# Performance work log

Measured on AMD Instinct MI355X. Metric: run time of the kernel, lower is better.

## Reference

```python
import jax, jax.numpy as jnp
import numpy as np

D = 1024; H = 8; QLR = 384; KVLR = 256; NOPE = 128; ROPE = 64; VD = 128
E = 8; TOPK = 2; INTER = 512; NSH = 2; B = 2; T = 2048
QKD = NOPE + ROPE  # 192


def _rms(x, w, eps=1e-6):
    return x * jax.lax.rsqrt(jnp.mean(x * x, axis=-1, keepdims=True) + eps) * w


def _rope(x, cos, sin):
    # x: [B,T,h,ROPE]; pairs are consecutive elements (torch view(...,-1,2)).
    x0 = x[..., 0::2]
    x1 = x[..., 1::2]
    c = cos[None, :, None, :]
    s = sin[None, :, None, :]
    y0 = x0 * c - x1 * s
    y1 = x0 * s + x1 * c
    return jnp.stack([y0, y1], axis=-1).reshape(x.shape)


def setup_inputs() -> dict:
    key = jax.random.key(0)
    ks = jax.random.split(key, 12)
    def w(k, shape, scale=0.02):
        return jax.random.normal(k, shape, dtype=jnp.float32) * scale
    inv = 1.0 / (10000.0 ** (jnp.arange(0, ROPE, 2, dtype=jnp.float32) / ROPE))
    ang = jnp.arange(T, dtype=jnp.float32)[:, None] * inv[None, :]  # [T, ROPE//2]
    return {
        "x": jax.random.normal(ks[0], (B, T, D), dtype=jnp.float32),
        "freqs_cos": jnp.cos(ang),
        "freqs_sin": jnp.sin(ang),
        "rmsn1_w": jnp.ones((D,), jnp.float32),
        "rmsn2_w": jnp.ones((D,), jnp.float32),
        "latent_w": w(ks[1], (D, QLR + KVLR + ROPE)),
        "q_norm_w": jnp.ones((QLR,), jnp.float32),
        "q_up_w": w(ks[2], (QLR, H * QKD)),
        "kv_norm_w": jnp.ones((KVLR,), jnp.float32),
        "kv_up_w": w(ks[3], (KVLR, H * (NOPE + VD))),
        "c_proj_w": w(ks[4], (D, D)),
        "gate_w": w(ks[5], (D, E)),
        "sh_w1": w(ks[6], (D, INTER * NSH)),
        "sh_w2": w(ks[7], (INTER * NSH, D)),
        "sh_w3": w(ks[8], (D, INTER * NSH)),
        "e_w1": w(ks[9], (E, D, INTER)),
        "e_w2": w(ks[10], (E, INTER, D)),
        "e_w3": w(ks[11], (E, D, INTER)),
    }


def reference(x, freqs_cos, freqs_sin, rmsn1_w, rmsn2_w, latent_w, q_norm_w,
              q_up_w, kv_norm_w, kv_up_w, c_proj_w, gate_w, sh_w1, sh_w2,
              sh_w3, e_w1, e_w2, e_w3):
    Bx, Tx, _ = x.shape
    # ---- MLA attention ----
    h = _rms(x, rmsn1_w)
    lat = h @ latent_w
    q_l, kv_l, k_r = jnp.split(lat, [QLR, QLR + KVLR], axis=-1)
    q = (_rms(q_l, q_norm_w) @ q_up_w).reshape(Bx, Tx, H, QKD)
    q_n, q_r = q[..., :NOPE], q[..., NOPE:]
    q_r = _rope(q_r, freqs_cos, freqs_sin)
    q = jnp.concatenate([q_n, q_r], axis=-1)  # [B,T,H,QKD]
    kv = (_rms(kv_l, kv_norm_w) @ kv_up_w).reshape(Bx, Tx, H, NOPE + VD)
    k_n, v = kv[..., :NOPE], kv[..., NOPE:]
    k_r = _rope(k_r[:, :, None, :], freqs_cos, freqs_sin)
    k_r = jnp.broadcast_to(k_r, (Bx, Tx, H, ROPE))
    k = jnp.concatenate([k_n, k_r], axis=-1)
    scale = 1.0 / jnp.sqrt(jnp.float32(QKD))
    scores = jnp.einsum('bqhd,bkhd->bhqk', q, k) * scale
    causal = jnp.tril(jnp.ones((Tx, Tx), dtype=bool))
    scores = jnp.where(causal, scores, jnp.finfo(scores.dtype).min)
    attn = jax.nn.softmax(scores, axis=-1)
    y = jnp.einsum('bhqk,bkhd->bqhd', attn, v).reshape(Bx, Tx, D)
    x = x + y @ c_proj_w
    # ---- DeepSeekMoE ----
    h2 = _rms(x, rmsn2_w).reshape(-1, D)  # [N, D]
    y_sh = (jax.nn.silu(h2 @ sh_w1) * (h2 @ sh_w3)) @ sh_w2
    scores_g = jax.nn.softmax(h2 @ gate_w, axis=-1)  # [N, E]
    w_top, idx = jax.lax.top_k(scores_g, TOPK)  # weights == gathered original scores
    # combine weights per expert (route_scale = 1.0)
    cw = jnp.sum(jax.nn.one_hot(idx, E, dtype=h2.dtype) * w_top[..., None], axis=1)  # [N, E]
    h1 = jnp.einsum('nd,edi->eni', h2, e_w1)
    h3 = jnp.einsum('nd,edi->eni', h2, e_w3)
    out_e = jnp.einsum('eni,eid->end', jax.nn.silu(h1) * h3, e_w2)  # [E, N, D]
    y_moe = y_sh + jnp.einsum('end,ne->nd', out_e, cw)
    return x + y_moe.reshape(Bx, Tx, D)
```

## Files before the change

### kernel.cpp

```cpp
#include <hip/hip_runtime.h>
#include <hip/hip_bf16.h>
#include <math.h>

#define D_ 1024
#define H_ 8
#define QLR_ 384
#define KVLR_ 256
#define NOPE_ 128
#define ROPE_ 64
#define VD_ 128
#define E_ 8
#define INTER_ 512
#define B_ 2
#define T_ 2048
#define QKD_ 192
#define NTOK (B_*T_)
#define LSTR 4608
#define MAXMB 72

typedef __attribute__((ext_vector_type(8))) short short8;
typedef __attribute__((ext_vector_type(4))) float f32x4;

__device__ __forceinline__ unsigned short f2bf(float f) {
  union { float f; unsigned u; } v; v.f = f;
  return (unsigned short)((v.u + 0x7FFFu + ((v.u >> 16) & 1u)) >> 16);
}
__device__ __forceinline__ float bf2f(unsigned short h) {
  union { unsigned u; float f; } v; v.u = ((unsigned)h) << 16;
  return v.f;
}

#define GLD16(SRC, DST) __builtin_amdgcn_global_load_lds( \
    (__attribute__((address_space(1))) void*)(SRC), \
    (__attribute__((address_space(3))) void*)(DST), 16, 0, 0)

#define DPPF(v, ctrl) __int_as_float(__builtin_amdgcn_update_dpp(0, __float_as_int(v), ctrl, 0xF, 0xF, true))
__device__ __forceinline__ float dppmax16(float v) {
  v = fmaxf(v, DPPF(v, 0xB1));
  v = fmaxf(v, DPPF(v, 0x4E));
  v = fmaxf(v, DPPF(v, 0x124));
  v = fmaxf(v, DPPF(v, 0x128));
  return v;
}
__device__ __forceinline__ float dppsum16(float v) {
  v += DPPF(v, 0xB1);
  v += DPPF(v, 0x4E);
  v += DPPF(v, 0x124);
  v += DPPF(v, 0x128);
  return v;
}

__global__ __launch_bounds__(256) void transpose_f32_bf16(
    const float* __restrict__ in, unsigned short* __restrict__ out,
    int R, int C, size_t inBS, size_t outBS) {
  __shared__ float tile[32][33];
  const float* inp = in + (size_t)blockIdx.z * inBS;
  unsigned short* outp = out + (size_t)blockIdx.z * outBS;
  int c0 = blockIdx.x * 32, r0 = blockIdx.y * 32;
  int tx = threadIdx.x & 31, ty = threadIdx.x >> 5;
  #pragma unroll
  for (int i = 0; i < 4; ++i) {
    int rr = ty + i * 8;
    tile[rr][tx] = inp[(size_t)(r0 + rr) * C + c0 + tx];
  }
  __syncthreads();
  #pragma unroll
  for (int i = 0; i < 4; ++i) {
    int rr = ty + i * 8;
    outp[(size_t)(c0 + rr) * R + r0 + tx] = f2bf(tile[tx][rr]);
  }
}

__global__ __launch_bounds__(256) void transpose_pair(
    const float* __restrict__ in1, const float* __restrict__ in3,
    unsigned short* __restrict__ out, int K, int C1, size_t inBS, size_t outBS) {
  __shared__ float tile[32][33];
  int z = blockIdx.z; int bat = z >> 1; int f = (z & 1) * 16;
  const float* src = ((z & 1) ? in3 : in1) + (size_t)bat * inBS;
  unsigned short* o = out + (size_t)bat * outBS;
  int c0 = blockIdx.x * 32, r0 = blockIdx.y * 32;
  int tx = threadIdx.x & 31, ty = threadIdx.x >> 5;
  #pragma unroll
  for (int i = 0; i < 4; ++i) {
    int rr = ty + i * 8;
    tile[rr][tx] = src[(size_t)(r0 + rr) * C1 + c0 + tx];
  }
  __syncthreads();
  #pragma unroll
  for (int i = 0; i < 4; ++i) {
    int cc = ty + i * 8;
    int c = c0 + cc;
    int n = ((c >> 4) << 5) + (c & 15) + f;
    o[(size_t)n * K + r0 + tx] = f2bf(tile[tx][cc]);
  }
}

template<typename TI>
__global__ __launch_bounds__(256) void rms_to_bf16(
    const TI* __restrict__ src, int stride, int off, const float* __restrict__ w,
    unsigned short* __restrict__ out, int Dd, int outStride) {
  int row = blockIdx.x;
  const TI* xr = src + (size_t)row * stride + off;
  float ss = 0.f;
  for (int i = threadIdx.x; i < Dd; i += 256) {
    float v;
    if constexpr (sizeof(TI) == 2) v = bf2f((unsigned short)xr[i]); else v = (float)xr[i];
    ss += v * v;
  }
  for (int o = 1; o < 64; o <<= 1) ss += __shfl_xor(ss, o);
  __shared__ float red[4];
  if ((threadIdx.x & 63) == 0) red[threadIdx.x >> 6] = ss;
  __syncthreads();
  float tot = red[0] + red[1] + red[2] + red[3];
  float inv = 1.f / sqrtf(tot / Dd + 1e-6f);
  for (int i = threadIdx.x; i < Dd; i += 256) {
    float v;
    if constexpr (sizeof(TI) == 2) v = bf2f((unsigned short)xr[i]); else v = (float)xr[i];
    out[(size_t)row * outStride + i] = f2bf(v * inv * w[i]);
  }
}

__global__ __launch_bounds__(256) void lat_post(
    const unsigned short* __restrict__ lat, const float* __restrict__ qw,
    const float* __restrict__ kw, const float* __restrict__ fc, const float* __restrict__ fs,
    unsigned short* __restrict__ qn, unsigned short* __restrict__ kvn,
    unsigned short* __restrict__ kr) {
  int row = blockIdx.x, tid = threadIdx.x;
  int lane = tid & 63, wv = tid >> 6;
  const unsigned short* lr = lat + (size_t)row * 768;
  float s1 = 0.f, s2 = 0.f;
  for (int i = tid; i < QLR_; i += 256) { float v = bf2f(lr[i]); s1 += v * v; }
  { float v = bf2f(lr[QLR_ + tid]); s2 = v * v; }
  for (int o = 1; o < 64; o <<= 1) { s1 += __shfl_xor(s1, o); s2 += __shfl_xor(s2, o); }
  __shared__ float red[8];
  if (lane == 0) { red[wv] = s1; red[4 + wv] = s2; }
  __syncthreads();
  float inv1 = 1.f / sqrtf((red[0] + red[1] + red[2] + red[3]) / QLR_ + 1e-6f);
  float inv2 = 1.f / sqrtf((red[4] + red[5] + red[6] + red[7]) / KVLR_ + 1e-6f);
  for (int i = tid; i < QLR_; i += 256)
    qn[(size_t)row * QLR_ + i] = f2bf(bf2f(lr[i]) * inv1 * qw[i]);
  kvn[(size_t)row * KVLR_ + tid] = f2bf(bf2f(lr[QLR_ + tid]) * inv2 * kw[tid]);
  if (tid < 32) {
    int t = row & (T_ - 1);
    float c = fc[t * 32 + tid], s = fs[t * 32 + tid];
    float x0 = bf2f(lr[640 + 2 * tid]), x1 = bf2f(lr[640 + 2 * tid + 1]);
    kr[(size_t)row * ROPE_ + 2 * tid]     = f2bf(x0 * c - x1 * s);
    kr[(size_t)row * ROPE_ + 2 * tid + 1] = f2bf(x0 * s + x1 * c);
  }
}

template<int MODE>
__global__ __launch_bounds__(256) void gemm_bf16(
    const unsigned short* __restrict__ A, const unsigned short* __restrict__ Bt,
    void* __restrict__ Cv, int M, int N, int K,
    const float* __restrict__ addv) {
  __shared__ __align__(16) unsigned short As[128 * 32];
  __shared__ __align__(16) unsigned short Bs[128 * 32];
  const int tid = threadIdx.x;
  const int lane = tid & 63, wave = tid >> 6;
  const int wm = wave >> 1, wn = wave & 1;
  const int bm = blockIdx.y * 128, bn = blockIdx.x * 128;
  const int r = lane & 15, g = lane >> 4;

  f32x4 acc[4][4];
  #pragma unroll
  for (int i = 0; i < 4; ++i)
    #pragma unroll
    for (int j = 0; j < 4; ++j) acc[i][j] = (f32x4)0.f;

  const int rl0 = wave * 16 + (lane >> 2);
  const int rl1 = rl0 + 64;
  const int kc = (lane & 3) * 8;
  char* AsB = (char*)As; char* BsB = (char*)Bs;

  for (int k0 = 0; k0 < K; k0 += 32) {
    GLD16(A + (size_t)(bm + rl0) * K + k0 + kc, AsB + wave * 1024);
    GLD16(A + (size_t)(bm + rl1) * K + k0 + kc, AsB + (wave + 4) * 1024);
    GLD16(Bt + (size_t)(bn + rl0) * K + k0 + kc, BsB + wave * 1024);
    GLD16(Bt + (size_t)(bn + rl1) * K + k0 + kc, BsB + (wave + 4) * 1024);
    __syncthreads();
    short8 af[4], bfr[4];
    #pragma unroll
    for (int mi = 0; mi < 4; ++mi)
      af[mi] = *(const short8*)(As + (wm * 64 + mi * 16 + r) * 32 + g * 8);
    #pragma unroll
    for (int nj = 0; nj < 4; ++nj)
      bfr[nj] = *(const short8*)(Bs + (wn * 64 + nj * 16 + r) * 32 + g * 8);
    #pragma unroll
    for (int mi = 0; mi < 4; ++mi)
      #pragma unroll
      for (int nj = 0; nj < 4; ++nj)
        acc[mi][nj] = __builtin_amdgcn_mfma_f32_16x16x32_bf16(af[mi], bfr[nj], acc[mi][nj], 0, 0, 0);
    __syncthreads();
  }

  const int orow0 = wm * 64 + g * 4;
  const int ocol0 = bn + wn * 64 + r;
  #pragma unroll
  for (int mi = 0; mi < 4; ++mi) {
    #pragma unroll
    for (int reg = 0; reg < 4; ++reg) {
      int mrow = bm + orow0 + mi * 16 + reg;
      if (MODE == 4) {
        unsigned short* C = (unsigned short*)Cv;
        size_t bas2 = (size_t)mrow * (N >> 1) + ((bn + wn * 64) >> 1) + r;
        #pragma unroll
        for (int p = 0; p < 2; ++p) {
          float a = acc[mi][2 * p][reg], b3 = acc[mi][2 * p + 1][reg];
          C[bas2 + p * 16] = f2bf((a / (1.f + __expf(-a))) * b3);
        }
      } else {
        size_t bas = (size_t)mrow * N + ocol0;
        if (MODE == 0) {
          unsigned short* C = (unsigned short*)Cv;
          #pragma unroll
          for (int nj = 0; nj < 4; ++nj) C[bas + nj * 16] = f2bf(acc[mi][nj][reg]);
        } else if (MODE == 1) {
          float* C = (float*)Cv;
          #pragma unroll
          for (int nj = 0; nj < 4; ++nj) C[bas + nj * 16] = acc[mi][nj][reg] + addv[bas + nj * 16];
        } else {
          float* C = (float*)Cv;
          #pragma unroll
          for (int nj = 0; nj < 4; ++nj) C[bas + nj * 16] += acc[mi][nj][reg];
        }
      }
    }
  }
}

__global__ __launch_bounds__(256) void gemm_moe13(
    const unsigned short* __restrict__ A, const unsigned short* __restrict__ W,
    unsigned short* __restrict__ Cb,
    const int* __restrict__ lists, const int* __restrict__ map, const int* __restrict__ sbase) {
  int mb = map[blockIdx.y];
  if (mb < 0) return;
  const int e = mb >> 16, ib = mb & 0xFFFF;
  __shared__ __align__(16) unsigned short As[128 * 32];
  __shared__ __align__(16) unsigned short Bs[128 * 32];
  const int tid = threadIdx.x, lane = tid & 63, wave = tid >> 6;
  const int wm = wave >> 1, wn = wave & 1;
  const int bn = blockIdx.x * 128;
  const int r = lane & 15, g = lane >> 4;

  f32x4 acc[4][4];
  #pragma unroll
  for (int i = 0; i < 4; ++i)
    #pragma unroll
    for (int j = 0; j < 4; ++j) acc[i][j] = (f32x4)0.f;

  const int rl0 = wave * 16 + (lane >> 2), rl1 = rl0 + 64;
  const int kc = (lane & 3) * 8;
  int t0 = lists[e * LSTR + ib * 128 + rl0]; if (t0 < 0) t0 = 0;
  int t1 = lists[e * LSTR + ib * 128 + rl1]; if (t1 < 0) t1 = 0;
  const unsigned short* Wb = W + (size_t)e * 1024 * 1024;
  char* AsB = (char*)As; char* BsB = (char*)Bs;

  for (int k0 = 0; k0 < 1024; k0 += 32) {
    GLD16(A + (size_t)t0 * 1024 + k0 + kc, AsB + wave * 1024);
    GLD16(A + (size_t)t1 * 1024 + k0 + kc, AsB + (wave + 4) * 1024);
    GLD16(Wb + (size_t)(bn + rl0) * 1024 + k0 + kc, BsB + wave * 1024);
    GLD16(Wb + (size_t)(bn + rl1) * 1024 + k0 + kc, BsB + (wave + 4) * 1024);
    __syncthreads();
    short8 af[4], bfr[4];
    #pragma unroll
    for (int mi = 0; mi < 4; ++mi)
      af[mi] = *(const short8*)(As + (wm * 64 + mi * 16 + r) * 32 + g * 8);
    #pragma unroll
    for (int nj = 0; nj < 4; ++nj)
      bfr[nj] = *(const short8*)(Bs + (wn * 64 + nj * 16 + r) * 32 + g * 8);
    #pragma unroll
    for (int mi = 0; mi < 4; ++mi)
      #pragma unroll
      for (int nj = 0; nj < 4; ++nj)
        acc[mi][nj] = __builtin_amdgcn_mfma_f32_16x16x32_bf16(af[mi], bfr[nj], acc[mi][nj], 0, 0, 0);
    __syncthreads();
  }
  const int sb = sbase[e] + ib * 128;
  const int hc = ((bn + wn * 64) >> 1) + r;
  #pragma unroll
  for (int mi = 0; mi < 4; ++mi)
    #pragma unroll
    for (int reg = 0; reg < 4; ++reg) {
      int srow = sb + wm * 64 + mi * 16 + g * 4 + reg;
      #pragma unroll
      for (int p = 0; p < 2; ++p) {
        float a = acc[mi][2 * p][reg], b3 = acc[mi][2 * p + 1][reg];
        Cb[(size_t)srow * 512 + hc + p * 16] = f2bf((a / (1.f + __expf(-a))) * b3);
      }
    }
}

__global__ __launch_bounds__(256) void gemm_moe2(
    const unsigned short* __restrict__ Am, const unsigned short* __restrict__ W,
    float* __restrict__ out,
    const int* __restrict__ lists, const int* __restrict__ map, const int* __restrict__ sbase,
    const float* __restrict__ cw) {
  int mb = map[blockIdx.y];
  if (mb < 0) return;
  const int e = mb >> 16, ib = mb & 0xFFFF;
  __shared__ __align__(16) unsigned short As[128 * 32];
  __shared__ __align__(16) unsigned short Bs[128 * 32];
  const int tid = threadIdx.x, lane = tid & 63, wave = tid >> 6;
  const int wm = wave >> 1, wn = wave & 1;
  const int bn = blockIdx.x * 128;
  const int r = lane & 15, g = lane >> 4;

  f32x4 acc[4][4];
  #pragma unroll
  for (int i = 0; i < 4; ++i)
    #pragma unroll
    for (int j = 0; j < 4; ++j) acc[i][j] = (f32x4)0.f;

  const int rl0 = wave * 16 + (lane >> 2), rl1 = rl0 + 64;
  const int kc = (lane & 3) * 8;
  const int sb = sbase[e] + ib * 128;
  const unsigned short* Wb = W + (size_t)e * 512 * 1024;
  char* AsB = (char*)As; char* BsB = (char*)Bs;

  for (int k0 = 0; k0 < 512; k0 += 32) {
    GLD16(Am + (size_t)(sb + rl0) * 512 + k0 + kc, AsB + wave * 1024);
    GLD16(Am + (size_t)(sb + rl1) * 512 + k0 + kc, AsB + (wave + 4) * 1024);
    GLD16(Wb + (size_t)(bn + rl0) * 512 + k0 + kc, BsB + wave * 1024);
    GLD16(Wb + (size_t)(bn + rl1) * 512 + k0 + kc, BsB + (wave + 4) * 1024);
    __syncthreads();
    short8 af[4], bfr[4];
    #pragma unroll
    for (int mi = 0; mi < 4; ++mi)
      af[mi] = *(const short8*)(As + (wm * 64 + mi * 16 + r) * 32 + g * 8);
    #pragma unroll
    for (int nj = 0; nj < 4; ++nj)
      bfr[nj] = *(const short8*)(Bs + (wn * 64 + nj * 16 + r) * 32 + g * 8);
    #pragma unroll
    for (int mi = 0; mi < 4; ++mi)
      #pragma unroll
      for (int nj = 0; nj < 4; ++nj)
        acc[mi][nj] = __builtin_amdgcn_mfma_f32_16x16x32_bf16(af[mi], bfr[nj], acc[mi][nj], 0, 0, 0);
    __syncthreads();
  }
  const int ocol0 = bn + wn * 64 + r;
  #pragma unroll
  for (int mi = 0; mi < 4; ++mi)
    #pragma unroll
    for (int reg = 0; reg < 4; ++reg) {
      int orow = wm * 64 + mi * 16 + g * 4 + reg;
      int tok = lists[e * LSTR + ib * 128 + orow];
      if (tok >= 0) {
        float wt = cw[(size_t)tok * E_ + e];
        #pragma unroll
        for (int nj = 0; nj < 4; ++nj)
          atomicAdd(out + (size_t)tok * 1024 + ocol0 + nj * 16, acc[mi][nj][reg] * wt);
      }
    }
}

__global__ void rope_q_bf16(unsigned short* __restrict__ q, const float* __restrict__ c_,
                            const float* __restrict__ s_) {
  int idx = blockIdx.x * blockDim.x + threadIdx.x;
  if (idx >= NTOK * H_ * 32) return;
  int i = idx & 31, h = (idx >> 5) & 7, n = idx >> 8;
  int t = n & (T_ - 1);
  float c = c_[t * 32 + i], s = s_[t * 32 + i];
  unsigned short* base = q + (size_t)n * (H_ * QKD_) + h * QKD_ + NOPE_;
  float x0 = bf2f(base[2 * i]), x1 = bf2f(base[2 * i + 1]);
  base[2 * i]     = f2bf(x0 * c - x1 * s);
  base[2 * i + 1] = f2bf(x0 * s + x1 * c);
}

__global__ __launch_bounds__(256) void vtrans(const unsigned short* __restrict__ kvb,
                                              unsigned short* __restrict__ vt) {
  __shared__ unsigned short tile[32][33];
  int bh = blockIdx.z; int b = bh >> 3, h = bh & 7;
  int t0 = blockIdx.x * 32, d0 = blockIdx.y * 32;
  int tx = threadIdx.x & 31, ty = threadIdx.x >> 5;
  #pragma unroll
  for (int i = 0; i < 4; ++i) {
    int row = ty + i * 8;
    tile[row][tx] = kvb[((size_t)(b * T_ + t0 + row) * H_ + h) * 256 + 128 + d0 + tx];
  }
  __syncthreads();
  #pragma unroll
  for (int i = 0; i < 4; ++i) {
    int row = ty + i * 8;
    vt[((size_t)bh * 128 + d0 + row) * T_ + t0 + tx] = tile[tx][row];
  }
}

#define AQ 64
#define AK 32
#define VP 40
__global__ __launch_bounds__(256) void attn_mfma(
    const unsigned short* __restrict__ q,
    const unsigned short* __restrict__ kv,
    const unsigned short* __restrict__ kr,
    const unsigned short* __restrict__ vt,
    unsigned short* __restrict__ y) {
  __shared__ __align__(16) unsigned short Qs[AQ * 192];
  __shared__ __align__(16) unsigned short Ks[AK * 192];
  __shared__ __align__(16) unsigned short Vl[128 * VP];
  __shared__ __align__(16) unsigned short Ps[4 * 16 * VP];
  const int tid = threadIdx.x, lane = tid & 63, wave = tid >> 6;
  const int r = lane & 15, g = lane >> 4;
  const int bh = blockIdx.y, b = bh >> 3, h = bh & 7;
  const int qt = gridDim.x - 1 - blockIdx.x;
  const int q0 = qt * AQ;
  const size_t bT = (size_t)b * T_;
  const unsigned short* vbase = vt + (size_t)bh * 128 * T_;
  char* QsB = (char*)Qs; char* KsB = (char*)Ks;

  #pragma unroll
  for (int it = 0; it < 6; ++it) {
    int c = tid + it * 256;
    int row = c / 24, c8 = c % 24;
    short8 v = *(const short8*)(q + ((bT + q0 + row) * H_ + h) * 192 + c8 * 8);
    *(short8*)(QsB + ((row * 384 + c8 * 16) ^ ((row & 7) << 4))) = v;
  }

  float m_i[4], l_i[4];
  f32x4 o[8];
  #pragma unroll
  for (int i = 0; i < 4; ++i) { m_i[i] = -1e30f; l_i[i] = 0.f; }
  #pragma unroll
  for (int cb = 0; cb < 8; ++cb) o[cb] = (f32x4)0.f;

  const float scale = 0.07216878364870322f;
  const int ntiles = q0 / AK + 2;

  short8 kreg[3], vreg[2];
  int krow[3], kcol[3];
  #pragma unroll
  for (int it = 0; it < 3; ++it) {
    int c = tid + it * 256;
    krow[it] = c / 24; kcol[it] = c % 24;
    kreg[it] = (kcol[it] < 16)
      ? *(const short8*)(kv + ((bT + krow[it]) * H_ + h) * 256 + kcol[it] * 8)
      : *(const short8*)(kr + (bT + krow[it]) * 64 + (kcol[it] - 16) * 8);
  }
  #pragma unroll
  for (int it = 0; it < 2; ++it) {
    int x = tid + it * 256;
    vreg[it] = *(const short8*)(vbase + (size_t)(x >> 2) * T_ + (x & 3) * 8);
  }

  for (int kt = 0; kt < ntiles; ++kt) {
    __syncthreads();
    #pragma unroll
    for (int it = 0; it < 3; ++it)
      *(short8*)(KsB + ((krow[it] * 384 + kcol[it] * 16) ^ ((krow[it] & 7) << 4))) = kreg[it];
    #pragma unroll
    for (int it = 0; it < 2; ++it) {
      int x = tid + it * 256;
      *(short8*)(Vl + (x >> 2) * VP + (x & 3) * 8) = vreg[it];
    }
    __syncthreads();

    if (kt + 1 < ntiles) {
      int k1 = (kt + 1) * AK;
      #pragma unroll
      for (int it = 0; it < 3; ++it)
        kreg[it] = (kcol[it] < 16)
          ? *(const short8*)(kv + ((bT + k1 + krow[it]) * H_ + h) * 256 + kcol[it] * 8)
          : *(const short8*)(kr + (bT + k1 + krow[it]) * 64 + (kcol[it] - 16) * 8);
      #pragma unroll
      for (int it = 0; it < 2; ++it) {
        int x = tid + it * 256;
        vreg[it] = *(const short8*)(vbase + (size_t)(x >> 2) * T_ + k1 + (x & 3) * 8);
      }
    }

    const int k0 = kt * AK;
    f32x4 sf0 = (f32x4)0.f, sf1 = (f32x4)0.f;
    {
      int qrow = wave * 16 + r;
      int qsw = (qrow & 7) << 4, ksw = (r & 7) << 4;
      #pragma unroll
      for (int kk = 0; kk < 6; ++kk) {
        short8 aq = *(const short8*)(QsB + ((qrow * 384 + kk * 64 + g * 16) ^ qsw));
        short8 b0 = *(const short8*)(KsB + ((r * 384 + kk * 64 + g * 16) ^ ksw));
        short8 b1 = *(const short8*)(KsB + (((16 + r) * 384 + kk * 64 + g * 16) ^ ksw));
        sf0 = __builtin_amdgcn_mfma_f32_16x16x32_bf16(aq, b0, sf0, 0, 0, 0);
        sf1 = __builtin_amdgcn_mfma_f32_16x16x32_bf16(aq, b1, sf1, 0, 0, 0);
      }
    }
    float fac[4];
    bool needs = false;
    #pragma unroll
    for (int reg = 0; reg < 4; ++reg) {
      float s0 = sf0[reg] * scale;
      float s1 = sf1[reg] * scale;
      int qp = q0 + wave * 16 + g * 4 + reg;
      if (k0 + r > qp) s0 = -1e30f;
      if (k0 + 16 + r > qp) s1 = -1e30f;
      float mt = dppmax16(fmaxf(s0, s1));
      float fc, mn;
      if (mt > m_i[reg] + 5.f) {
        mn = mt; fc = __expf(m_i[reg] - mn); m_i[reg] = mn; needs = true;
      } else { mn = m_i[reg]; fc = 1.f; }
      float e0 = __expf(s0 - mn), e1 = __expf(s1 - mn);
      float rs = dppsum16(e0 + e1);
      l_i[reg] = l_i[reg] * fc + rs;
      fac[reg] = fc;
      int prow = g * 4 + reg;
      Ps[wave * 16 * VP + prow * VP + r] = f2bf(e0);
      Ps[wave * 16 * VP + prow * VP + 16 + r] = f2bf(e1);
    }
    if (__any(needs)) {
      #pragma unroll
      for (int cb = 0; cb < 8; ++cb)
        #pragma unroll
        for (int reg = 0; reg < 4; ++reg) o[cb][reg] *= fac[reg];
    }
    short8 pa = *(const short8*)(Ps + wave * 16 * VP + r * VP + g * 8);
    #pragma unroll
    for (int cb = 0; cb < 8; ++cb) {
      short8 vb = *(const short8*)(Vl + (cb * 16 + r) * VP + g * 8);
      o[cb] = __builtin_amdgcn_mfma_f32_16x16x32_bf16(pa, vb, o[cb], 0, 0, 0);
    }
  }

  #pragma unroll
  for (int reg = 0; reg < 4; ++reg) {
    float inv = 1.f / l_i[reg];
    int nrow = q0 + wave * 16 + g * 4 + reg;
    size_t bas = (bT + nrow) * (size_t)D_ + h * VD_;
    #pragma unroll
    for (int cb = 0; cb < 8; ++cb)
      y[bas + cb * 16 + r] = f2bf(o[cb][reg] * inv);
  }
}

__global__ __launch_bounds__(256) void rms2_gate(
    const float* __restrict__ xo, const float* __restrict__ rw, const float* __restrict__ gw,
    unsigned short* __restrict__ h2b, float* __restrict__ cw) {
  int row = blockIdx.x, tid = threadIdx.x;
  int lane = tid & 63, wv = tid >> 6;
  const float* xr = xo + (size_t)row * D_;
  float v[4]; float ss = 0.f;
  #pragma unroll
  for (int j = 0; j < 4; ++j) { v[j] = xr[tid + j * 256]; ss += v[j] * v[j]; }
  for (int o = 1; o < 64; o <<= 1) ss += __shfl_xor(ss, o);
  __shared__ float red[4];
  if (lane == 0) red[wv] = ss;
  __syncthreads();
  float inv = 1.f / sqrtf((red[0] + red[1] + red[2] + red[3]) / D_ + 1e-6f);
  float a[E_] = {0, 0, 0, 0, 0, 0, 0, 0};
  #pragma unroll
  for (int j = 0; j < 4; ++j) {
    int i = tid + j * 256;
    float hv = v[j] * inv * rw[i];
    h2b[(size_t)row * D_ + i] = f2bf(hv);
    const float* wr = gw + (size_t)i * E_;
    #pragma unroll
    for (int e = 0; e < E_; ++e) a[e] += hv * wr[e];
  }
  #pragma unroll
  for (int e = 0; e < E_; ++e) {
    float t = a[e];
    for (int o = 1; o < 64; o <<= 1) t += __shfl_xor(t, o);
    a[e] = t;
  }
  __shared__ float ga[4][E_];
  if (lane == 0)
    #pragma unroll
    for (int e = 0; e < E_; ++e) ga[wv][e] = a[e];
  __syncthreads();
  if (tid == 0) {
    float lg[E_];
    #pragma unroll
    for (int e = 0; e < E_; ++e) lg[e] = ga[0][e] + ga[1][e] + ga[2][e] + ga[3][e];
    float mx = lg[0];
    #pragma unroll
    for (int e = 1; e < E_; ++e) mx = fmaxf(mx, lg[e]);
    float sum = 0.f; float p[E_];
    #pragma unroll
    for (int e = 0; e < E_; ++e) { p[e] = __expf(lg[e] - mx); sum += p[e]; }
    float is = 1.f / sum;
    int i1 = 0; float b1 = p[0];
    #pragma unroll
    for (int e = 1; e < E_; ++e) if (p[e] > b1) { b1 = p[e]; i1 = e; }
    int i2 = -1; float b2 = -1.f;
    #pragma unroll
    for (int e = 0; e < E_; ++e) if (e != i1 && p[e] > b2) { b2 = p[e]; i2 = e; }
    #pragma unroll
    for (int e = 0; e < E_; ++e)
      cw[(size_t)row * E_ + e] = (e == i1) ? b1 * is : (e == i2 ? b2 * is : 0.f);
  }
}

__global__ __launch_bounds__(256) void moe_build(const float* __restrict__ cw,
                                                 int* __restrict__ lists, int* __restrict__ counts) {
  int e = blockIdx.x, tid = threadIdx.x;
  int lane = tid & 63, wv = tid >> 6;
  __shared__ int wsum[4];
  __shared__ int base;
  if (tid == 0) base = 0;
  __syncthreads();
  for (int c0 = 0; c0 < NTOK; c0 += 256) {
    int tok = c0 + tid;
    bool f = cw[(size_t)tok * E_ + e] > 0.f;
    unsigned long long m = __ballot(f);
    int pos = __popcll(m & ((1ull << lane) - 1ull));
    if (lane == 0) wsum[wv] = __popcll(m);
    __syncthreads();
    int woff = base;
    #pragma unroll
    for (int w = 0; w < 4; ++w) if (w < wv) woff += wsum[w];
    if (f) lists[e * LSTR + woff + pos] = tok;
    __syncthreads();
    if (tid == 0) base += wsum[0] + wsum[1] + wsum[2] + wsum[3];
    __syncthreads();
  }
  int cnt = base;
  int padded = (cnt + 127) & ~127;
  for (int i2 = cnt + tid; i2 < padded; i2 += 256) lists[e * LSTR + i2] = -1;
  if (tid == 0) { counts[e] = cnt; counts[8 + e] = padded >> 7; }
}

__global__ void moe_finalize(const int* __restrict__ counts, int* __restrict__ map,
                             int* __restrict__ sbase) {
  if (threadIdx.x == 0 && blockIdx.x == 0) {
    int cum = 0;
    for (int e = 0; e < E_; ++e) {
      sbase[e] = cum * 128;
      int nb = counts[8 + e];
      for (int i = 0; i < nb; ++i) map[cum + i] = (e << 16) | i;
      cum += nb;
    }
    for (; cum < MAXMB; ++cum) map[cum] = -1;
  }
}

extern "C" void kernel_launch(void* const* d_in, const int* in_sizes, int n_in,
                              void* d_out, int out_size, void* d_ws, size_t ws_size,
                              hipStream_t stream) {
  const float* x        = (const float*)d_in[0];
  const float* fcos     = (const float*)d_in[1];
  const float* fsin     = (const float*)d_in[2];
  const float* rmsn1_w  = (const float*)d_in[3];
  const float* rmsn2_w  = (const float*)d_in[4];
  const float* latent_w = (const float*)d_in[5];
  const float* q_norm_w = (const float*)d_in[6];
  const float* q_up_w   = (const float*)d_in[7];
  const float* kv_norm_w= (const float*)d_in[8];
  const float* kv_up_w  = (const float*)d_in[9];
  const float* c_proj_w = (const float*)d_in[10];
  const float* gate_w   = (const float*)d_in[11];
  const float* sh_w1    = (const float*)d_in[12];
  const float* sh_w2    = (const float*)d_in[13];
  const float* sh_w3    = (const float*)d_in[14];
  const float* e_w1     = (const float*)d_in[15];
  const float* e_w2     = (const float*)d_in[16];
  const float* e_w3     = (const float*)d_in[17];
  float* out = (float*)d_out;

  char* base = (char*)d_ws;
  size_t off = 0;
  auto take = [&](size_t bytes) { char* p = base + off; off += (bytes + 255) & ~(size_t)255; return p; };
  unsigned short* Wlat  = (unsigned short*)take((size_t)768 * 1024 * 2);
  unsigned short* Wqup  = (unsigned short*)take((size_t)1536 * 384 * 2);
  unsigned short* Wkv   = (unsigned short*)take((size_t)2048 * 256 * 2);
  unsigned short* Wcp   = (unsigned short*)take((size_t)1024 * 1024 * 2);
  unsigned short* Wsh13 = (unsigned short*)take((size_t)2048 * 1024 * 2);
  unsigned short* Wsh2  = (unsigned short*)take((size_t)1024 * 1024 * 2);
  unsigned short* Wew13 = (unsigned short*)take((size_t)8 * 1024 * 1024 * 2);
  unsigned short* Wew2  = (unsigned short*)take((size_t)8 * 1024 * 512 * 2);
  float* cw             = (float*)take((size_t)NTOK * E_ * 4);
  int* lists            = (int*)take((size_t)E_ * LSTR * 4);
  int* counts           = (int*)take(64 * 4);
  int* map              = (int*)take(MAXMB * 4);
  int* sbase            = (int*)take(E_ * 4);
  unsigned short* Vtg   = (unsigned short*)take((size_t)16 * 128 * T_ * 2);
  unsigned short* kr    = (unsigned short*)take((size_t)NTOK * 64 * 2);

  size_t actStart = off;
  size_t aoff = actStart;
  auto takeA = [&](size_t bytes) { char* p = base + aoff; aoff += (bytes + 255) & ~(size_t)255; return p; };
  unsigned short* h_bf = (unsigned short*)takeA((size_t)NTOK * 1024 * 2);
  unsigned short* lat  = (unsigned short*)takeA((size_t)NTOK * 768 * 2);
  unsigned short* qn   = (unsigned short*)takeA((size_t)NTOK * 384 * 2);
  unsigned short* kvn  = (unsigned short*)takeA((size_t)NTOK * 256 * 2);
  unsigned short* qq   = (unsigned short*)takeA((size_t)NTOK * 1536 * 2);
  unsigned short* kvb  = (unsigned short*)takeA((size_t)NTOK * 2048 * 2);
  unsigned short* y    = (unsigned short*)takeA((size_t)NTOK * 1024 * 2);

  size_t coff = actStart;
  auto takeC = [&](size_t bytes) { char* p = base + coff; coff += (bytes + 255) & ~(size_t)255; return p; };
  unsigned short* h2b  = (unsigned short*)takeC((size_t)NTOK * 1024 * 2);
  unsigned short* t1m  = (unsigned short*)takeC((size_t)NTOK * 1024 * 2);
  unsigned short* ehm  = (unsigned short*)takeC((size_t)9216 * 512 * 2);

  dim3 blk(256);

  transpose_f32_bf16<<<dim3(22, 32, 1), blk, 0, stream>>>(latent_w, Wlat, 1024, 704, 0, 0);
  transpose_f32_bf16<<<dim3(48, 12, 1), blk, 0, stream>>>(q_up_w, Wqup, 384, 1536, 0, 0);
  transpose_f32_bf16<<<dim3(64, 8, 1), blk, 0, stream>>>(kv_up_w, Wkv, 256, 2048, 0, 0);
  transpose_f32_bf16<<<dim3(32, 32, 1), blk, 0, stream>>>(c_proj_w, Wcp, 1024, 1024, 0, 0);
  transpose_f32_bf16<<<dim3(32, 32, 1), blk, 0, stream>>>(sh_w2, Wsh2, 1024, 1024, 0, 0);
  transpose_pair<<<dim3(32, 32, 2), blk, 0, stream>>>(sh_w1, sh_w3, Wsh13, 1024, 1024, 0, 0);
  transpose_pair<<<dim3(16, 32, 16), blk, 0, stream>>>(e_w1, e_w3, Wew13, 1024, 512,
      (size_t)1024 * 512, (size_t)1024 * 1024);
  transpose_f32_bf16<<<dim3(32, 16, 8), blk, 0, stream>>>(e_w2, Wew2, 512, 1024,
      (size_t)512 * 1024, (size_t)1024 * 512);

  rms_to_bf16<float><<<NTOK, blk, 0, stream>>>(x, D_, 0, rmsn1_w, h_bf, D_, D_);
  gemm_bf16<0><<<dim3(6, 32), blk, 0, stream>>>(h_bf, Wlat, lat, NTOK, 768, 1024, nullptr);
  lat_post<<<NTOK, blk, 0, stream>>>(lat, q_norm_w, kv_norm_w, fcos, fsin, qn, kvn, kr);
  gemm_bf16<0><<<dim3(12, 32), blk, 0, stream>>>(qn, Wqup, qq, NTOK, 1536, 384, nullptr);
  rope_q_bf16<<<(NTOK * H_ * 32 + 255) / 256, blk, 0, stream>>>(qq, fcos, fsin);
  gemm_bf16<0><<<dim3(16, 32), blk, 0, stream>>>(kvn, Wkv, kvb, NTOK, 2048, 256, nullptr);
  vtrans<<<dim3(T_/32, 4, 16), blk, 0, stream>>>(kvb, Vtg);
  attn_mfma<<<dim3(T_ / AQ, B_ * H_), blk, 0, stream>>>(qq, kvb, kr, Vtg, y);
  gemm_bf16<1><<<dim3(8, 32), blk, 0, stream>>>(y, Wcp, out, NTOK, 1024, 1024, x);
  rms2_gate<<<NTOK, blk, 0, stream>>>(out, rmsn2_w, gate_w, h2b, cw);
  moe_build<<<E_, blk, 0, stream>>>(cw, lists, counts);
  moe_finalize<<<1, 64, 0, stream>>>(counts, map, sbase);
  gemm_bf16<4><<<dim3(16, 32), blk, 0, stream>>>(h2b, Wsh13, t1m, NTOK, 2048, 1024, nullptr);
  gemm_bf16<2><<<dim3(8, 32), blk, 0, stream>>>(t1m, Wsh2, out, NTOK, 1024, 1024, nullptr);
  gemm_moe13<<<dim3(8, MAXMB), blk, 0, stream>>>(h2b, Wew13, ehm, lists, map, sbase);
  gemm_moe2<<<dim3(8, MAXMB), blk, 0, stream>>>(ehm, Wew2, out, lists, map, sbase, cw);
}
```

Before: 411.0 us.

## Fuse V transpose into kv GEMM, fuse q RoPE into attention, tune softmax

```diff
diff --git a/kernel.cpp b/kernel.cpp
--- a/kernel.cpp
+++ b/kernel.cpp
@@ -20,6 +20,7 @@
 
 typedef __attribute__((ext_vector_type(8))) short short8;
 typedef __attribute__((ext_vector_type(4))) float f32x4;
+typedef __attribute__((ext_vector_type(4))) unsigned short us4;
 
 __device__ __forceinline__ unsigned short f2bf(float f) {
   union { float f; unsigned u; } v; v.f = f;
@@ -153,7 +154,7 @@
 __global__ __launch_bounds__(256) void gemm_bf16(
     const unsigned short* __restrict__ A, const unsigned short* __restrict__ Bt,
     void* __restrict__ Cv, int M, int N, int K,
-    const float* __restrict__ addv) {
+    const float* __restrict__ addv, unsigned short* __restrict__ vtg) {
   __shared__ __align__(16) unsigned short As[128 * 32];
   __shared__ __align__(16) unsigned short Bs[128 * 32];
   const int tid = threadIdx.x;
@@ -192,6 +193,38 @@
       for (int nj = 0; nj < 4; ++nj)
         acc[mi][nj] = __builtin_amdgcn_mfma_f32_16x16x32_bf16(af[mi], bfr[nj], acc[mi][nj], 0, 0, 0);
     __syncthreads();
+  }
+
+  if (MODE == 5) {
+    unsigned short* C = (unsigned short*)Cv;
+    const int colbase = bn + wn * 64;
+    const int b = bm >> 11;
+    const int hh = colbase >> 8;
+    if ((colbase & 255) < 128) {
+      #pragma unroll
+      for (int mi = 0; mi < 4; ++mi)
+        #pragma unroll
+        for (int reg = 0; reg < 4; ++reg) {
+          int mrow = bm + wm * 64 + mi * 16 + g * 4 + reg;
+          size_t bas = (size_t)mrow * N + colbase + r;
+          #pragma unroll
+          for (int nj = 0; nj < 4; ++nj) C[bas + nj * 16] = f2bf(acc[mi][nj][reg]);
+        }
+    } else {
+      const int tl0 = (bm & 2047) + wm * 64 + g * 4;
+      const int d0 = (colbase & 255) - 128 + r;
+      #pragma unroll
+      for (int mi = 0; mi < 4; ++mi)
+        #pragma unroll
+        for (int nj = 0; nj < 4; ++nj) {
+          int d = d0 + nj * 16;
+          us4 pk;
+          #pragma unroll
+          for (int reg = 0; reg < 4; ++reg) pk[reg] = f2bf(acc[mi][nj][reg]);
+          *(us4*)(vtg + ((size_t)((b * 8 + hh) * 128 + d)) * 2048 + tl0 + mi * 16) = pk;
+        }
+    }
+    return;
   }
 
   const int orow0 = wm * 64 + g * 4;
@@ -354,38 +387,6 @@
     }
 }
 
-__global__ void rope_q_bf16(unsigned short* __restrict__ q, const float* __restrict__ c_,
-                            const float* __restrict__ s_) {
-  int idx = blockIdx.x * blockDim.x + threadIdx.x;
-  if (idx >= NTOK * H_ * 32) return;
-  int i = idx & 31, h = (idx >> 5) & 7, n = idx >> 8;
-  int t = n & (T_ - 1);
-  float c = c_[t * 32 + i], s = s_[t * 32 + i];
-  unsigned short* base = q + (size_t)n * (H_ * QKD_) + h * QKD_ + NOPE_;
-  float x0 = bf2f(base[2 * i]), x1 = bf2f(base[2 * i + 1]);
-  base[2 * i]     = f2bf(x0 * c - x1 * s);
-  base[2 * i + 1] = f2bf(x0 * s + x1 * c);
-}
-
-__global__ __launch_bounds__(256) void vtrans(const unsigned short* __restrict__ kvb,
-                                              unsigned short* __restrict__ vt) {
-  __shared__ unsigned short tile[32][33];
-  int bh = blockIdx.z; int b = bh >> 3, h = bh & 7;
-  int t0 = blockIdx.x * 32, d0 = blockIdx.y * 32;
-  int tx = threadIdx.x & 31, ty = threadIdx.x >> 5;
-  #pragma unroll
-  for (int i = 0; i < 4; ++i) {
-    int row = ty + i * 8;
-    tile[row][tx] = kvb[((size_t)(b * T_ + t0 + row) * H_ + h) * 256 + 128 + d0 + tx];
-  }
-  __syncthreads();
-  #pragma unroll
-  for (int i = 0; i < 4; ++i) {
-    int row = ty + i * 8;
-    vt[((size_t)bh * 128 + d0 + row) * T_ + t0 + tx] = tile[tx][row];
-  }
-}
-
 #define AQ 64
 #define AK 32
 #define VP 40
@@ -394,6 +395,7 @@
     const unsigned short* __restrict__ kv,
     const unsigned short* __restrict__ kr,
     const unsigned short* __restrict__ vt,
+    const float* __restrict__ fcos, const float* __restrict__ fsin,
     unsigned short* __restrict__ y) {
   __shared__ __align__(16) unsigned short Qs[AQ * 192];
   __shared__ __align__(16) unsigned short Ks[AK * 192];
@@ -413,6 +415,17 @@
     int c = tid + it * 256;
     int row = c / 24, c8 = c % 24;
     short8 v = *(const short8*)(q + ((bT + q0 + row) * H_ + h) * 192 + c8 * 8);
+    if (c8 >= 16) {
+      int t = q0 + row;
+      int ib = (c8 - 16) * 4;
+      #pragma unroll
+      for (int p = 0; p < 4; ++p) {
+        float cc = fcos[t * 32 + ib + p], sn = fsin[t * 32 + ib + p];
+        float x0 = bf2f((unsigned short)v[2 * p]), x1 = bf2f((unsigned short)v[2 * p + 1]);
+        v[2 * p]     = (short)f2bf(x0 * cc - x1 * sn);
+        v[2 * p + 1] = (short)f2bf(x0 * sn + x1 * cc);
+      }
+    }
     *(short8*)(QsB + ((row * 384 + c8 * 16) ^ ((row & 7) << 4))) = v;
   }
 
@@ -423,7 +436,7 @@
   #pragma unroll
   for (int cb = 0; cb < 8; ++cb) o[cb] = (f32x4)0.f;
 
-  const float scale = 0.07216878364870322f;
+  const float scale2 = 0.07216878364870322f * 1.44269504088896f;
   const int ntiles = q0 / AK + 2;
 
   short8 kreg[3], vreg[2];
@@ -473,6 +486,7 @@
     {
       int qrow = wave * 16 + r;
       int qsw = (qrow & 7) << 4, ksw = (r & 7) << 4;
+      __builtin_amdgcn_s_setprio(1);
       #pragma unroll
       for (int kk = 0; kk < 6; ++kk) {
         short8 aq = *(const short8*)(QsB + ((qrow * 384 + kk * 64 + g * 16) ^ qsw));
@@ -481,28 +495,31 @@
         sf0 = __builtin_amdgcn_mfma_f32_16x16x32_bf16(aq, b0, sf0, 0, 0, 0);
         sf1 = __builtin_amdgcn_mfma_f32_16x16x32_bf16(aq, b1, sf1, 0, 0, 0);
       }
+      __builtin_amdgcn_s_setprio(0);
     }
     float fac[4];
     bool needs = false;
     #pragma unroll
     for (int reg = 0; reg < 4; ++reg) {
-      float s0 = sf0[reg] * scale;
-      float s1 = sf1[reg] * scale;
+      float s0 = sf0[reg] * scale2;
+      float s1 = sf1[reg] * scale2;
       int qp = q0 + wave * 16 + g * 4 + reg;
       if (k0 + r > qp) s0 = -1e30f;
       if (k0 + 16 + r > qp) s1 = -1e30f;
       float mt = dppmax16(fmaxf(s0, s1));
-      float fc, mn;
-      if (mt > m_i[reg] + 5.f) {
-        mn = mt; fc = __expf(m_i[reg] - mn); m_i[reg] = mn; needs = true;
-      } else { mn = m_i[reg]; fc = 1.f; }
-      float e0 = __expf(s0 - mn), e1 = __expf(s1 - mn);
+      float fc = 1.f, mn = m_i[reg];
+      if (mt > mn + 8.f) {
+        mn = mt; fc = exp2f(m_i[reg] - mn); m_i[reg] = mn; needs = true;
+      }
+      float e0 = exp2f(s0 - mn), e1 = exp2f(s1 - mn);
       float rs = dppsum16(e0 + e1);
       l_i[reg] = l_i[reg] * fc + rs;
       fac[reg] = fc;
+      __hip_bfloat162 pk = __float22bfloat162_rn(float2{e0, e1});
+      unsigned u = *(unsigned*)&pk;
       int prow = g * 4 + reg;
-      Ps[wave * 16 * VP + prow * VP + r] = f2bf(e0);
-      Ps[wave * 16 * VP + prow * VP + 16 + r] = f2bf(e1);
+      Ps[wave * 16 * VP + prow * VP + r] = (unsigned short)u;
+      Ps[wave * 16 * VP + prow * VP + 16 + r] = (unsigned short)(u >> 16);
     }
     if (__any(needs)) {
       #pragma unroll
@@ -511,11 +528,13 @@
         for (int reg = 0; reg < 4; ++reg) o[cb][reg] *= fac[reg];
     }
     short8 pa = *(const short8*)(Ps + wave * 16 * VP + r * VP + g * 8);
+    __builtin_amdgcn_s_setprio(1);
     #pragma unroll
     for (int cb = 0; cb < 8; ++cb) {
       short8 vb = *(const short8*)(Vl + (cb * 16 + r) * VP + g * 8);
       o[cb] = __builtin_amdgcn_mfma_f32_16x16x32_bf16(pa, vb, o[cb], 0, 0, 0);
     }
+    __builtin_amdgcn_s_setprio(0);
   }
 
   #pragma unroll
@@ -703,19 +722,17 @@
       (size_t)512 * 1024, (size_t)1024 * 512);
 
   rms_to_bf16<float><<<NTOK, blk, 0, stream>>>(x, D_, 0, rmsn1_w, h_bf, D_, D_);
-  gemm_bf16<0><<<dim3(6, 32), blk, 0, stream>>>(h_bf, Wlat, lat, NTOK, 768, 1024, nullptr);
+  gemm_bf16<0><<<dim3(6, 32), blk, 0, stream>>>(h_bf, Wlat, lat, NTOK, 768, 1024, nullptr, nullptr);
   lat_post<<<NTOK, blk, 0, stream>>>(lat, q_norm_w, kv_norm_w, fcos, fsin, qn, kvn, kr);
-  gemm_bf16<0><<<dim3(12, 32), blk, 0, stream>>>(qn, Wqup, qq, NTOK, 1536, 384, nullptr);
-  rope_q_bf16<<<(NTOK * H_ * 32 + 255) / 256, blk, 0, stream>>>(qq, fcos, fsin);
-  gemm_bf16<0><<<dim3(16, 32), blk, 0, stream>>>(kvn, Wkv, kvb, NTOK, 2048, 256, nullptr);
-  vtrans<<<dim3(T_/32, 4, 16), blk, 0, stream>>>(kvb, Vtg);
-  attn_mfma<<<dim3(T_ / AQ, B_ * H_), blk, 0, stream>>>(qq, kvb, kr, Vtg, y);
-  gemm_bf16<1><<<dim3(8, 32), blk, 0, stream>>>(y, Wcp, out, NTOK, 1024, 1024, x);
+  gemm_bf16<0><<<dim3(12, 32), blk, 0, stream>>>(qn, Wqup, qq, NTOK, 1536, 384, nullptr, nullptr);
+  gemm_bf16<5><<<dim3(16, 32), blk, 0, stream>>>(kvn, Wkv, kvb, NTOK, 2048, 256, nullptr, Vtg);
+  attn_mfma<<<dim3(T_ / AQ, B_ * H_), blk, 0, stream>>>(qq, kvb, kr, Vtg, fcos, fsin, y);
+  gemm_bf16<1><<<dim3(8, 32), blk, 0, stream>>>(y, Wcp, out, NTOK, 1024, 1024, x, nullptr);
   rms2_gate<<<NTOK, blk, 0, stream>>>(out, rmsn2_w, gate_w, h2b, cw);
   moe_build<<<E_, blk, 0, stream>>>(cw, lists, counts);
   moe_finalize<<<1, 64, 0, stream>>>(counts, map, sbase);
-  gemm_bf16<4><<<dim3(16, 32), blk, 0, stream>>>(h2b, Wsh13, t1m, NTOK, 2048, 1024, nullptr);
-  gemm_bf16<2><<<dim3(8, 32), blk, 0, stream>>>(t1m, Wsh2, out, NTOK, 1024, 1024, nullptr);
+  gemm_bf16<4><<<dim3(16, 32), blk, 0, stream>>>(h2b, Wsh13, t1m, NTOK, 2048, 1024, nullptr, nullptr);
+  gemm_bf16<2><<<dim3(8, 32), blk, 0, stream>>>(t1m, Wsh2, out, NTOK, 1024, 1024, nullptr, nullptr);
   gemm_moe13<<<dim3(8, MAXMB), blk, 0, stream>>>(h2b, Wew13, ehm, lists, map, sbase);
   gemm_moe2<<<dim3(8, MAXMB), blk, 0, stream>>>(ehm, Wew2, out, lists, map, sbase, cw);
 }
```

New measurement: 410.3 us. No clear change (-0.2%).
